# Optimization experiments

Measured on AMD Instinct MI355X. Metric: run time of the kernel, lower is better.

The kernel has to match this reference:

```python
import jax, jax.numpy as jnp
import numpy as np


def _mlp(h, W_in, b_in, W_hid, b_hid, W_out, b_out):
    # 392 -> 1000 -> (1000)x4 -> 392, ReLU between linear layers (NICE shift net)
    h = jax.nn.relu(h @ W_in + b_in)
    for i in range(W_hid.shape[0]):  # fixed small layer count, not a data dim
        h = jax.nn.relu(h @ W_hid[i] + b_hid[i])
    return h @ W_out + b_out


def setup_inputs() -> dict:
    key = jax.random.key(0)
    ks = jax.random.split(key, 4)
    B, D, MID = 4096, 784, 1000
    half = D // 2
    return {
        "x": jax.random.normal(ks[0], (B, D), jnp.float32),
        "log_det_J": jnp.zeros((1,), jnp.float32),
        "W_in": jax.random.normal(ks[1], (half, MID), jnp.float32) * 0.05,
        "b_in": jnp.zeros((MID,), jnp.float32),
        "W_hid": jax.random.normal(ks[2], (4, MID, MID), jnp.float32) * 0.03,
        "b_hid": jnp.zeros((4, MID), jnp.float32),
        "W_out": jax.random.normal(ks[3], (MID, half), jnp.float32) * 0.03,
        "b_out": jnp.zeros((half,), jnp.float32),
    }


def reference(x, log_det_J, W_in, b_in, W_hid, b_hid, W_out, b_out):
    # mask_config = 0: first = even columns, second = odd columns
    first = x[:, 0::2]   # (B, D/2)
    second = x[:, 1::2]  # (B, D/2)
    shift = _mlp(first, W_in, b_in, W_hid, b_hid, W_out, b_out)
    y_second = second + shift  # coupling_law (reverse=False)
    # interleave: y[:, 0::2] = first, y[:, 1::2] = y_second, in one strided write
    y = jnp.stack([first, y_second], axis=2).reshape(x.shape)
    return (y, log_det_J)
```

## Files before the change

kernel.cpp:

```cpp
#include <hip/hip_runtime.h>

typedef __bf16 bf16;
typedef __bf16 bf16x8 __attribute__((ext_vector_type(8)));
typedef float f32x4 __attribute__((ext_vector_type(4)));

#define M_TOT 4096
#define D_IN  784
#define HALF  392
#define MID   1000
#define K0PAD 448
#define NPAD  1024
#define N5PAD 512

__device__ __forceinline__ void g2l16(const bf16* g, bf16* l) {
  __builtin_amdgcn_global_load_lds(
      (__attribute__((address_space(1))) void*)(g),
      (__attribute__((address_space(3))) void*)(l),
      16, 0, 0);
}

__global__ void pack_first_k(const float* __restrict__ x, bf16* __restrict__ A0) {
  int k = blockIdx.x * 256 + threadIdx.x;
  int m = blockIdx.y;
  if (k < K0PAD)
    A0[(size_t)m * K0PAD + k] = (k < HALF) ? (bf16)x[(size_t)m * D_IN + 2 * k] : (bf16)0.f;
}

__global__ void prep_weights_k(const float* __restrict__ W_in,
                               const float* __restrict__ W_hid,
                               const float* __restrict__ W_out,
                               bf16* __restrict__ WT0, bf16* __restrict__ WTh,
                               bf16* __restrict__ WT5) {
  int t = blockIdx.x;
  const float* W; bf16* WT; int K, N, Kpad, tn, tk;
  if (t < 448) {
    W = W_in; WT = WT0; K = HALF; N = MID; Kpad = K0PAD;
    tn = t & 31; tk = t >> 5;
  } else if (t < 448 + 4096) {
    int u = t - 448; int i = u >> 10; u &= 1023;
    W = W_hid + (size_t)i * MID * MID; WT = WTh + (size_t)i * NPAD * NPAD;
    K = MID; N = MID; Kpad = NPAD;
    tn = u & 31; tk = u >> 5;
  } else {
    int u = t - 4544;
    W = W_out; WT = WT5; K = MID; N = HALF; Kpad = NPAD;
    tn = u & 15; tk = u >> 4;
  }
  __shared__ float tb[32][33];
  int n0 = tn * 32, k0 = tk * 32;
  int tx = threadIdx.x, ty = threadIdx.y;
#pragma unroll
  for (int r = 0; r < 4; ++r) {
    int k = k0 + ty + 8 * r, n = n0 + tx;
    tb[ty + 8 * r][tx] = (k < K && n < N) ? W[(size_t)k * N + n] : 0.f;
  }
  __syncthreads();
#pragma unroll
  for (int r = 0; r < 4; ++r) {
    int n = n0 + ty + 8 * r, k = k0 + tx;
    WT[(size_t)n * Kpad + k] = (bf16)tb[tx][ty + 8 * r];
  }
}

template <int BN, int EPI>
__global__ __launch_bounds__(256, 1)
void gemm_k(const bf16* __restrict__ A, const bf16* __restrict__ BT,
            const float* __restrict__ bias, int bias_n,
            bf16* __restrict__ C,
            const float* __restrict__ x, float* __restrict__ y,
            int K) {
  constexpr int BM = 128, BK = 64;
  constexpr int WN = BN / 2, NT = WN / 16;
  __shared__ bf16 ldsA[BM * BK];
  __shared__ bf16 ldsB[BN * BK];
  const int tid = threadIdx.x, wave = tid >> 6, lane = tid & 63;
  const int bn = blockIdx.x, bm = blockIdx.y;

  const int srow = lane >> 3;
  const int sqz = (lane & 7) ^ srow;
  const bf16* gA = A + ((size_t)bm * BM + wave * (BM / 4) + srow) * K + sqz * 8;
  const bf16* gB = BT + ((size_t)bn * BN + wave * (BN / 4) + srow) * K + sqz * 8;
  bf16* lA = &ldsA[wave * (BM / 4) * BK];
  bf16* lB = &ldsB[wave * (BN / 4) * BK];

  const int mlane = lane & 15, quad = lane >> 4;
  const int wm = (wave & 1) * 64, wn = (wave >> 1) * WN;
  const int axor = mlane & 7;
  const bf16* raBase = &ldsA[(wm + mlane) * BK];
  const bf16* rbBase = &ldsB[(wn + mlane) * BK];

  f32x4 acc[4][NT] = {};

  const int KT = K >> 6;
#pragma unroll
  for (int i = 0; i < BM / 32; ++i) g2l16(gA + (size_t)(8 * i) * K, lA + (8 * i) * BK);
#pragma unroll
  for (int i = 0; i < BN / 32; ++i) g2l16(gB + (size_t)(8 * i) * K, lB + (8 * i) * BK);

  for (int kt = 0; kt < KT; ++kt) {
    __syncthreads();
    bf16x8 af[2][4], bfr[2][NT];
#pragma unroll
    for (int s = 0; s < 2; ++s) {
      const int co = ((s * 4 + quad) ^ axor) * 8;
#pragma unroll
      for (int i = 0; i < 4; ++i) af[s][i] = *(const bf16x8*)(raBase + i * 16 * BK + co);
#pragma unroll
      for (int i = 0; i < NT; ++i) bfr[s][i] = *(const bf16x8*)(rbBase + i * 16 * BK + co);
    }
    __syncthreads();
    if (kt + 1 < KT) {
      const size_t off = (size_t)(kt + 1) * BK;
#pragma unroll
      for (int i = 0; i < BM / 32; ++i) g2l16(gA + off + (size_t)(8 * i) * K, lA + (8 * i) * BK);
#pragma unroll
      for (int i = 0; i < BN / 32; ++i) g2l16(gB + off + (size_t)(8 * i) * K, lB + (8 * i) * BK);
    }
#pragma unroll
    for (int s = 0; s < 2; ++s)
#pragma unroll
      for (int mt = 0; mt < 4; ++mt)
#pragma unroll
        for (int nt = 0; nt < NT; ++nt)
          acc[mt][nt] = __builtin_amdgcn_mfma_f32_16x16x32_bf16(
              af[s][mt], bfr[s][nt], acc[mt][nt], 0, 0, 0);
  }

  const int ng0 = bn * BN + wn + mlane;
  const int mg0 = bm * BM + wm + quad * 4;

  if (EPI == 0) {
    float bv[NT];
#pragma unroll
    for (int nt = 0; nt < NT; ++nt) {
      int n = ng0 + nt * 16;
      bv[nt] = (n < bias_n) ? bias[n] : 0.f;
    }
#pragma unroll
    for (int mt = 0; mt < 4; ++mt)
#pragma unroll
      for (int nt = 0; nt < NT; ++nt)
#pragma unroll
        for (int r = 0; r < 4; ++r) {
          int m = mg0 + mt * 16 + r;
          int n = ng0 + nt * 16;
          float v = fmaxf(acc[mt][nt][r] + bv[nt], 0.f);
          C[(size_t)m * NPAD + n] = (bf16)v;
        }
  } else {
    const float2* x2 = (const float2*)x;
    float2* y2 = (float2*)y;
#pragma unroll
    for (int nt = 0; nt < NT; ++nt) {
      int n = ng0 + nt * 16;
      if (n < HALF) {
        float bb = bias[n];
#pragma unroll
        for (int mt = 0; mt < 4; ++mt)
#pragma unroll
          for (int r = 0; r < 4; ++r) {
            int m = mg0 + mt * 16 + r;
            size_t off = (size_t)m * (D_IN / 2) + n;
            float2 v = x2[off];
            v.y += acc[mt][nt][r] + bb;
            y2[off] = v;
          }
      }
    }
  }
}

extern "C" void kernel_launch(void* const* d_in, const int* in_sizes, int n_in,
                              void* d_out, int out_size, void* d_ws, size_t ws_size,
                              hipStream_t stream) {
  const float* x     = (const float*)d_in[0];
  const float* ldj   = (const float*)d_in[1];
  const float* W_in  = (const float*)d_in[2];
  const float* b_in  = (const float*)d_in[3];
  const float* W_hid = (const float*)d_in[4];
  const float* b_hid = (const float*)d_in[5];
  const float* W_out = (const float*)d_in[6];
  const float* b_out = (const float*)d_in[7];
  float* y = (float*)d_out;

  char* p = (char*)d_ws;
  bf16* A0  = (bf16*)(p + 0);
  bf16* H0  = (bf16*)(p + 3670016);
  bf16* H1  = (bf16*)(p + 12058624);
  bf16* WT0 = (bf16*)(p + 20447232);
  bf16* WTh = (bf16*)(p + 21364736);
  bf16* WT5 = (bf16*)(p + 29753344);

  pack_first_k<<<dim3(2, M_TOT), 256, 0, stream>>>(x, A0);
  prep_weights_k<<<dim3(5056), dim3(32, 8), 0, stream>>>(W_in, W_hid, W_out, WT0, WTh, WT5);

  gemm_k<128, 0><<<dim3(8, 32), 256, 0, stream>>>(A0, WT0, b_in, MID, H0, nullptr, nullptr, K0PAD);
  gemm_k<128, 0><<<dim3(8, 32), 256, 0, stream>>>(H0, WTh + 0 * (size_t)NPAD * NPAD, b_hid + 0 * MID, MID, H1, nullptr, nullptr, NPAD);
  gemm_k<128, 0><<<dim3(8, 32), 256, 0, stream>>>(H1, WTh + 1 * (size_t)NPAD * NPAD, b_hid + 1 * MID, MID, H0, nullptr, nullptr, NPAD);
  gemm_k<128, 0><<<dim3(8, 32), 256, 0, stream>>>(H0, WTh + 2 * (size_t)NPAD * NPAD, b_hid + 2 * MID, MID, H1, nullptr, nullptr, NPAD);
  gemm_k<128, 0><<<dim3(8, 32), 256, 0, stream>>>(H1, WTh + 3 * (size_t)NPAD * NPAD, b_hid + 3 * MID, MID, H0, nullptr, nullptr, NPAD);
  gemm_k<64, 1><<<dim3(8, 32), 256, 0, stream>>>(H0, WT5, b_out, HALF, nullptr, x, y, NPAD);

  hipMemcpyAsync(y + (size_t)M_TOT * D_IN, ldj, sizeof(float), hipMemcpyDeviceToDevice, stream);
}
```

Measured before the change: 203.9 us.

## Shrink GEMM M-tile to 64, template K, and merge prep kernels

Merges the input packing, weight transpose and log-det copy into one prep launch, which removes two launches and a memcpy. The GEMM M tile drops from 128 to 64, doubling the grid from 256 to 512 blocks so all CUs on the MI355X get work. K becomes a compile-time constant so the loop can be fully resolved, and launch bounds allow two blocks per CU. Smaller tiles mean less reuse of each B tile and more global traffic per FLOP.

```diff
diff --git a/kernel.cpp b/kernel.cpp
--- a/kernel.cpp
+++ b/kernel.cpp
@@ -19,19 +19,24 @@
       16, 0, 0);
 }
 
-__global__ void pack_first_k(const float* __restrict__ x, bf16* __restrict__ A0) {
-  int k = blockIdx.x * 256 + threadIdx.x;
-  int m = blockIdx.y;
-  if (k < K0PAD)
-    A0[(size_t)m * K0PAD + k] = (k < HALF) ? (bf16)x[(size_t)m * D_IN + 2 * k] : (bf16)0.f;
-}
-
-__global__ void prep_weights_k(const float* __restrict__ W_in,
-                               const float* __restrict__ W_hid,
-                               const float* __restrict__ W_out,
-                               bf16* __restrict__ WT0, bf16* __restrict__ WTh,
-                               bf16* __restrict__ WT5) {
-  int t = blockIdx.x;
+__global__ void prep_k(const float* __restrict__ x, const float* __restrict__ ldj,
+                       const float* __restrict__ W_in, const float* __restrict__ W_hid,
+                       const float* __restrict__ W_out,
+                       bf16* __restrict__ A0, bf16* __restrict__ WT0,
+                       bf16* __restrict__ WTh, bf16* __restrict__ WT5,
+                       float* __restrict__ y) {
+  int b = blockIdx.x;
+  int tid = threadIdx.x;
+  if (b == 0 && tid == 0) y[(size_t)M_TOT * D_IN] = ldj[0];
+
+  if (b < 8192) {
+    int m = b >> 1;
+    int k = (b & 1) * 256 + tid;
+    if (k < K0PAD)
+      A0[(size_t)m * K0PAD + k] = (k < HALF) ? (bf16)x[(size_t)m * D_IN + 2 * k] : (bf16)0.f;
+    return;
+  }
+  int t = b - 8192;
   const float* W; bf16* WT; int K, N, Kpad, tn, tk;
   if (t < 448) {
     W = W_in; WT = WT0; K = HALF; N = MID; Kpad = K0PAD;
@@ -48,7 +53,7 @@
   }
   __shared__ float tb[32][33];
   int n0 = tn * 32, k0 = tk * 32;
-  int tx = threadIdx.x, ty = threadIdx.y;
+  int tx = tid & 31, ty = tid >> 5;
 #pragma unroll
   for (int r = 0; r < 4; ++r) {
     int k = k0 + ty + 8 * r, n = n0 + tx;
@@ -62,36 +67,35 @@
   }
 }
 
-template <int BN, int EPI>
-__global__ __launch_bounds__(256, 1)
+template <int BM, int BN, int EPI, int K>
+__global__ __launch_bounds__(256, 2)
 void gemm_k(const bf16* __restrict__ A, const bf16* __restrict__ BT,
             const float* __restrict__ bias, int bias_n,
             bf16* __restrict__ C,
-            const float* __restrict__ x, float* __restrict__ y,
-            int K) {
-  constexpr int BM = 128, BK = 64;
-  constexpr int WN = BN / 2, NT = WN / 16;
+            const float* __restrict__ x, float* __restrict__ y) {
+  constexpr int BK = 64;
+  constexpr int MT = BM / 32, NT = BN / 32;
+  constexpr int KT = K / BK;
   __shared__ bf16 ldsA[BM * BK];
   __shared__ bf16 ldsB[BN * BK];
   const int tid = threadIdx.x, wave = tid >> 6, lane = tid & 63;
   const int bn = blockIdx.x, bm = blockIdx.y;
 
   const int srow = lane >> 3;
-  const int sqz = (lane & 7) ^ srow;
-  const bf16* gA = A + ((size_t)bm * BM + wave * (BM / 4) + srow) * K + sqz * 8;
-  const bf16* gB = BT + ((size_t)bn * BN + wave * (BN / 4) + srow) * K + sqz * 8;
+  const int sq = (lane & 7) ^ srow;
+  const bf16* gA = A + ((size_t)bm * BM + wave * (BM / 4) + srow) * K + sq * 8;
+  const bf16* gB = BT + ((size_t)bn * BN + wave * (BN / 4) + srow) * K + sq * 8;
   bf16* lA = &ldsA[wave * (BM / 4) * BK];
   bf16* lB = &ldsB[wave * (BN / 4) * BK];
 
   const int mlane = lane & 15, quad = lane >> 4;
-  const int wm = (wave & 1) * 64, wn = (wave >> 1) * WN;
+  const int wm = (wave & 1) * (BM / 2), wn = (wave >> 1) * (BN / 2);
   const int axor = mlane & 7;
   const bf16* raBase = &ldsA[(wm + mlane) * BK];
   const bf16* rbBase = &ldsB[(wn + mlane) * BK];
 
-  f32x4 acc[4][NT] = {};
-
-  const int KT = K >> 6;
+  f32x4 acc[MT][NT] = {};
+
 #pragma unroll
   for (int i = 0; i < BM / 32; ++i) g2l16(gA + (size_t)(8 * i) * K, lA + (8 * i) * BK);
 #pragma unroll
@@ -99,12 +103,12 @@
 
   for (int kt = 0; kt < KT; ++kt) {
     __syncthreads();
-    bf16x8 af[2][4], bfr[2][NT];
+    bf16x8 af[2][MT], bfr[2][NT];
 #pragma unroll
     for (int s = 0; s < 2; ++s) {
       const int co = ((s * 4 + quad) ^ axor) * 8;
 #pragma unroll
-      for (int i = 0; i < 4; ++i) af[s][i] = *(const bf16x8*)(raBase + i * 16 * BK + co);
+      for (int i = 0; i < MT; ++i) af[s][i] = *(const bf16x8*)(raBase + i * 16 * BK + co);
 #pragma unroll
       for (int i = 0; i < NT; ++i) bfr[s][i] = *(const bf16x8*)(rbBase + i * 16 * BK + co);
     }
@@ -119,7 +123,7 @@
 #pragma unroll
     for (int s = 0; s < 2; ++s)
 #pragma unroll
-      for (int mt = 0; mt < 4; ++mt)
+      for (int mt = 0; mt < MT; ++mt)
 #pragma unroll
         for (int nt = 0; nt < NT; ++nt)
           acc[mt][nt] = __builtin_amdgcn_mfma_f32_16x16x32_bf16(
@@ -137,7 +141,7 @@
       bv[nt] = (n < bias_n) ? bias[n] : 0.f;
     }
 #pragma unroll
-    for (int mt = 0; mt < 4; ++mt)
+    for (int mt = 0; mt < MT; ++mt)
 #pragma unroll
       for (int nt = 0; nt < NT; ++nt)
 #pragma unroll
@@ -156,7 +160,7 @@
       if (n < HALF) {
         float bb = bias[n];
 #pragma unroll
-        for (int mt = 0; mt < 4; ++mt)
+        for (int mt = 0; mt < MT; ++mt)
 #pragma unroll
           for (int r = 0; r < 4; ++r) {
             int m = mg0 + mt * 16 + r;
@@ -191,15 +195,13 @@
   bf16* WTh = (bf16*)(p + 21364736);
   bf16* WT5 = (bf16*)(p + 29753344);
 
-  pack_first_k<<<dim3(2, M_TOT), 256, 0, stream>>>(x, A0);
-  prep_weights_k<<<dim3(5056), dim3(32, 8), 0, stream>>>(W_in, W_hid, W_out, WT0, WTh, WT5);
-
-  gemm_k<128, 0><<<dim3(8, 32), 256, 0, stream>>>(A0, WT0, b_in, MID, H0, nullptr, nullptr, K0PAD);
-  gemm_k<128, 0><<<dim3(8, 32), 256, 0, stream>>>(H0, WTh + 0 * (size_t)NPAD * NPAD, b_hid + 0 * MID, MID, H1, nullptr, nullptr, NPAD);
-  gemm_k<128, 0><<<dim3(8, 32), 256, 0, stream>>>(H1, WTh + 1 * (size_t)NPAD * NPAD, b_hid + 1 * MID, MID, H0, nullptr, nullptr, NPAD);
-  gemm_k<128, 0><<<dim3(8, 32), 256, 0, stream>>>(H0, WTh + 2 * (size_t)NPAD * NPAD, b_hid + 2 * MID, MID, H1, nullptr, nullptr, NPAD);
-  gemm_k<128, 0><<<dim3(8, 32), 256, 0, stream>>>(H1, WTh + 3 * (size_t)NPAD * NPAD, b_hid + 3 * MID, MID, H0, nullptr, nullptr, NPAD);
-  gemm_k<64, 1><<<dim3(8, 32), 256, 0, stream>>>(H0, WT5, b_out, HALF, nullptr, x, y, NPAD);
-
-  hipMemcpyAsync(y + (size_t)M_TOT * D_IN, ldj, sizeof(float), hipMemcpyDeviceToDevice, stream);
-}
+  prep_k<<<dim3(8192 + 5056), 256, 0, stream>>>(x, ldj, W_in, W_hid, W_out,
+                                                A0, WT0, WTh, WT5, y);
+
+  gemm_k<64, 128, 0, K0PAD><<<dim3(8, 64), 256, 0, stream>>>(A0, WT0, b_in, MID, H0, nullptr, nullptr);
+  gemm_k<64, 128, 0, NPAD><<<dim3(8, 64), 256, 0, stream>>>(H0, WTh + 0 * (size_t)NPAD * NPAD, b_hid + 0 * MID, MID, H1, nullptr, nullptr);
+  gemm_k<64, 128, 0, NPAD><<<dim3(8, 64), 256, 0, stream>>>(H1, WTh + 1 * (size_t)NPAD * NPAD, b_hid + 1 * MID, MID, H0, nullptr, nullptr);
+  gemm_k<64, 128, 0, NPAD><<<dim3(8, 64), 256, 0, stream>>>(H0, WTh + 2 * (size_t)NPAD * NPAD, b_hid + 2 * MID, MID, H1, nullptr, nullptr);
+  gemm_k<64, 128, 0, NPAD><<<dim3(8, 64), 256, 0, stream>>>(H1, WTh + 3 * (size_t)NPAD * NPAD, b_hid + 3 * MID, MID, H0, nullptr, nullptr);
+  gemm_k<64, 64, 1, NPAD><<<dim3(8, 64), 256, 0, stream>>>(H0, WT5, b_out, HALF, nullptr, x, y);
+}
```

Result: faster. 183.9 us (-9.8%).
